# Kernel optimization log

Hardware: AMD Instinct MI355X
Metric: run time of the kernel (lower is better)

## Reference

```python
import jax, jax.numpy as jnp
import numpy as np

B, D, H, W = 1, 16, 16, 16
C, NH = 528, 8
HD = C // NH      # 66
K = 32            # retrieved memories per token


def setup_inputs() -> dict:
    key = jax.random.key(0)
    ks = jax.random.split(key, 4)
    x = jax.random.normal(ks[0], (B, D, H, W, C), jnp.float32)
    # simulated knn_memory.search output: (B, heads, N, K, 2[k/v], head_dim)
    knn_kv = jax.random.normal(ks[1], (B, NH, D * H * W, K, 2, HD), jnp.float32)
    w_qkv = jax.random.normal(ks[2], (3 * C, C), jnp.float32) * 0.02
    b_qkv = jnp.zeros((3 * C,), jnp.float32)
    w_proj = jax.random.normal(ks[3], (C, C), jnp.float32) * 0.02
    b_proj = jnp.zeros((C,), jnp.float32)
    return {"x": x, "knn_kv": knn_kv, "w_qkv": w_qkv, "b_qkv": b_qkv,
            "w_proj": w_proj, "b_proj": b_proj, "num_heads": NH}


def _l2norm(t):
    # F.normalize(t, dim=-1): t / max(||t||_2, eps)
    n = jnp.linalg.norm(t, axis=-1, keepdims=True)
    return t / jnp.maximum(n, 1e-12)


def _forward(x, knn_kv, w_qkv, b_qkv, w_proj, b_proj, num_heads):
    Bb, Dd, Hh, Ww, Cc = x.shape
    N = Dd * Hh * Ww
    hd = Cc // num_heads
    scaling = hd ** -0.5
    qkv = x.reshape(Bb * N, Cc) @ w_qkv.T + b_qkv
    qkv = qkv.reshape(Bb, N, 3, num_heads, hd).transpose(2, 0, 3, 1, 4)  # (3,B,h,N,hd)
    q, k, v = qkv[0], qkv[1], qkv[2]
    q = _l2norm(q)
    k = _l2norm(k)
    knn_k = knn_kv[..., 0, :]   # (B,h,N,K,hd)
    knn_v = knn_kv[..., 1, :]
    k_comb = jnp.concatenate([knn_k, k[..., None, :]], axis=-2)  # (B,h,N,K+1,hd)
    v_comb = jnp.concatenate([knn_v, v[..., None, :]], axis=-2)
    attn = jnp.einsum('bhnd,bhnkd->bhnk', q, k_comb) * scaling
    attn = jax.nn.softmax(attn, axis=-1)  # stable softmax
    out = jnp.einsum('bhnk,bhnkd->bhnd', attn, v_comb)  # (B,h,N,hd)
    out = out.transpose(0, 2, 1, 3).reshape(Bb * N, num_heads * hd)
    out = out @ w_proj.T + b_proj
    return out.reshape(Bb, Dd, Hh, Ww, Cc)


def reference(x, knn_kv, w_qkv, b_qkv, w_proj, b_proj, num_heads):
    return _forward(x, knn_kv, w_qkv, b_qkv, w_proj, b_proj, num_heads)
```

## Files before the change

kernel.cpp:

```cpp
#include <hip/hip_runtime.h>
#include <hip/hip_bf16.h>
#include <math.h>

#define N_POS 4096
#define C_DIM 528
#define NHEAD 8
#define HDIM  66
#define KNN   32
#define CQKV  1584
#define KP    544
#define NP1   1664
#define NP2   640

typedef __attribute__((ext_vector_type(8))) short short8;
typedef __attribute__((ext_vector_type(4))) float f32x4;
typedef __hip_bfloat16 bf16;

__global__ __launch_bounds__(256) void convpad3_kernel(
    const float* __restrict__ x, const float* __restrict__ wq,
    const float* __restrict__ wp,
    bf16* __restrict__ xb, bf16* __restrict__ wqb, bf16* __restrict__ wpb)
{
    int b = blockIdx.x;
    const float* src; bf16* dst; int Nr;
    if (b < N_POS)            { src = x;  dst = xb;  Nr = N_POS; }
    else if (b < N_POS + NP1) { b -= N_POS; src = wq; dst = wqb; Nr = CQKV; }
    else                      { b -= N_POS + NP1; src = wp; dst = wpb; Nr = C_DIM; }
    for (int c = threadIdx.x; c < KP; c += 256) {
        float v = (b < Nr && c < C_DIM) ? src[(size_t)b * C_DIM + c] : 0.0f;
        dst[(size_t)b * KP + c] = __float2bfloat16(v);
    }
}

__global__ __launch_bounds__(256) void gemm_mfma_kernel(
    const bf16* __restrict__ A, const bf16* __restrict__ B,
    const float* __restrict__ bias, float* __restrict__ C,
    int Nreal, int ldc)
{
    __shared__ short8 As[512];
    __shared__ short8 Bs[512];

    const int tid  = threadIdx.x;
    const int lane = tid & 63;
    const int wid  = tid >> 6;
    const int bm = blockIdx.y * 128;
    const int bn = blockIdx.x * 128;

    const int r0 = tid >> 2;
    const int c0 = tid & 3;
    const bf16* Ag = A + (size_t)(bm + r0) * KP + c0 * 8;
    const bf16* Bg = B + (size_t)(bn + r0) * KP + c0 * 8;
    const size_t roff = (size_t)64 * KP;

    short8 a0 = *(const short8*)(Ag);
    short8 a1 = *(const short8*)(Ag + roff);
    short8 b0 = *(const short8*)(Bg);
    short8 b1 = *(const short8*)(Bg + roff);

    const int w0 = r0 * 4 + (c0 ^ (r0 & 3));
    const int w1 = w0 + 256;

    const int wm = (wid >> 1) * 64;
    const int wn = (wid & 1) * 64;
    const int arow = wm + (lane & 15);
    const int brow = wn + (lane & 15);
    const int apc  = lane >> 4;
    const int aslot = arow * 4 + (apc ^ (arow & 3));
    const int bslot = brow * 4 + (apc ^ (brow & 3));

    f32x4 acc[4][4];
    #pragma unroll
    for (int i = 0; i < 4; ++i)
        #pragma unroll
        for (int j = 0; j < 4; ++j)
            acc[i][j] = (f32x4){0.f, 0.f, 0.f, 0.f};

    for (int k0 = 0;; k0 += 32) {
        As[w0] = a0; As[w1] = a1;
        Bs[w0] = b0; Bs[w1] = b1;
        __syncthreads();
        if (k0 + 32 < KP) {
            const bf16* An = Ag + (k0 + 32);
            const bf16* Bn = Bg + (k0 + 32);
            a0 = *(const short8*)(An);
            a1 = *(const short8*)(An + roff);
            b0 = *(const short8*)(Bn);
            b1 = *(const short8*)(Bn + roff);
        }
        short8 af[4], bfr[4];
        #pragma unroll
        for (int f = 0; f < 4; ++f) af[f]  = As[aslot + f * 64];
        #pragma unroll
        for (int f = 0; f < 4; ++f) bfr[f] = Bs[bslot + f * 64];
        #pragma unroll
        for (int i = 0; i < 4; ++i)
            #pragma unroll
            for (int j = 0; j < 4; ++j)
                acc[i][j] = __builtin_amdgcn_mfma_f32_16x16x32_bf16(
                    af[i], bfr[j], acc[i][j], 0, 0, 0);
        if (k0 + 32 >= KP) break;
        __syncthreads();
    }

    #pragma unroll
    for (int i = 0; i < 4; ++i) {
        const int row = bm + wm + i * 16 + (lane >> 4) * 4;
        #pragma unroll
        for (int j = 0; j < 4; ++j) {
            const int col = bn + wn + j * 16 + (lane & 15);
            if (col < Nreal) {
                const float bv = bias[col];
                #pragma unroll
                for (int r = 0; r < 4; ++r)
                    C[(size_t)(row + r) * ldc + col] = acc[i][j][r] + bv;
            }
        }
    }
}

__global__ __launch_bounds__(256) void attn_kernel(
    const float* __restrict__ qkv, const float* __restrict__ knn,
    bf16* __restrict__ out)
{
    const float scaling = 0.12309149097933272f;

    int bid = blockIdx.x;
    int h = bid >> 12;
    int n = bid & 4095;
    int tid = threadIdx.x;

    __shared__ float s_knn[KNN * 2 * HDIM];
    __shared__ float s_q[HDIM], s_k[HDIM], s_v[HDIM];
    __shared__ float s_dot[KNN + 1];
    __shared__ float s_scale[2];

    {
        const float4* src = (const float4*)(knn + ((size_t)bid) * (KNN * 2 * HDIM));
        float4* dst = (float4*)s_knn;
        for (int i = tid; i < KNN * 2 * HDIM / 4; i += 256) dst[i] = src[i];
    }
    const float* qp = qkv + (size_t)n * CQKV + h * HDIM;
    if (tid < HDIM) {
        s_q[tid] = qp[tid];
        s_k[tid] = qp[C_DIM + tid];
        s_v[tid] = qp[2 * C_DIM + tid];
    }
    __syncthreads();

    if (tid < 64) {
        float aq = s_q[tid] * s_q[tid];
        float ak = s_k[tid] * s_k[tid];
        if (tid < 2) {
            aq += s_q[64 + tid] * s_q[64 + tid];
            ak += s_k[64 + tid] * s_k[64 + tid];
        }
        #pragma unroll
        for (int off = 32; off; off >>= 1) {
            aq += __shfl_xor(aq, off);
            ak += __shfl_xor(ak, off);
        }
        if (tid == 0) {
            s_scale[0] = 1.0f / fmaxf(sqrtf(aq), 1e-12f);
            s_scale[1] = 1.0f / fmaxf(sqrtf(ak), 1e-12f);
        }
    }
    __syncthreads();
    if (tid < HDIM) {
        s_q[tid] *= s_scale[0];
        s_k[tid] *= s_scale[1];
    }
    __syncthreads();

    {
        int g = tid >> 3, l8 = tid & 7;
        float p = 0.f;
        for (int d = l8; d < HDIM; d += 8) p += s_q[d] * s_knn[g * (2 * HDIM) + d];
        p += __shfl_xor(p, 1);
        p += __shfl_xor(p, 2);
        p += __shfl_xor(p, 4);
        if (l8 == 0) s_dot[g] = p * scaling;
    }
    if (tid < 8) {
        float p = 0.f;
        for (int d = tid; d < HDIM; d += 8) p += s_q[d] * s_k[d];
        p += __shfl_xor(p, 1);
        p += __shfl_xor(p, 2);
        p += __shfl_xor(p, 4);
        if (tid == 0) s_dot[KNN] = p * scaling;
    }
    __syncthreads();

    if (tid < 64) {
        float x = (tid < 33) ? s_dot[tid] : -3.4e38f;
        float m = x;
        #pragma unroll
        for (int off = 32; off; off >>= 1) m = fmaxf(m, __shfl_xor(m, off));
        float e = (tid < 33) ? expf(x - m) : 0.f;
        float s = e;
        #pragma unroll
        for (int off = 32; off; off >>= 1) s += __shfl_xor(s, off);
        if (tid < 33) s_dot[tid] = e / s;
    }
    __syncthreads();

    if (tid < HDIM) {
        float acc = s_dot[KNN] * s_v[tid];
        #pragma unroll 8
        for (int k = 0; k < KNN; ++k)
            acc += s_dot[k] * s_knn[k * (2 * HDIM) + HDIM + tid];
        out[(size_t)n * KP + h * HDIM + tid] = __float2bfloat16(acc);
    }
    if (h == 0 && tid < KP - C_DIM) {
        out[(size_t)n * KP + C_DIM + tid] = __float2bfloat16(0.0f);
    }
}

extern "C" void kernel_launch(void* const* d_in, const int* in_sizes, int n_in,
                              void* d_out, int out_size, void* d_ws, size_t ws_size,
                              hipStream_t stream)
{
    const float* x      = (const float*)d_in[0];
    const float* knn_kv = (const float*)d_in[1];
    const float* w_qkv  = (const float*)d_in[2];
    const float* b_qkv  = (const float*)d_in[3];
    const float* w_proj = (const float*)d_in[4];
    const float* b_proj = (const float*)d_in[5];
    float* out = (float*)d_out;

    char* ws = (char*)d_ws;
    float* qkv = (float*)ws;
    bf16*  xb  = (bf16*)(ws + 25952256);
    bf16*  wqb = (bf16*)(ws + 25952256 + 4456448);
    bf16*  wpb = (bf16*)(ws + 25952256 + 4456448 + 1810432);
    bf16*  ab  = (bf16*)(ws + 25952256 + 4456448 + 1810432 + 696320);

    convpad3_kernel<<<N_POS + NP1 + NP2, 256, 0, stream>>>(x, w_qkv, w_proj, xb, wqb, wpb);

    gemm_mfma_kernel<<<dim3(NP1 / 128, N_POS / 128), 256, 0, stream>>>(
        xb, wqb, b_qkv, qkv, CQKV, CQKV);

    attn_kernel<<<dim3(NHEAD * N_POS), 256, 0, stream>>>(qkv, knn_kv, ab);

    gemm_mfma_kernel<<<dim3(NP2 / 128, N_POS / 128), 256, 0, stream>>>(
        ab, wpb, b_proj, out, C_DIM, C_DIM);
}
```

Baseline: 180.3 us.

## Process two tokens per attention block with register-staged KNN loads and fused normalization

Each attention block now handles two consecutive positions, with one 128-thread team per position, which halves the grid size. The KNN tile loads are issued into registers before being written to shared memory, so more loads are in flight at once. The L2 normalisation is folded algebraically into scale factors: the q·k dot, the norms and the local key dot are reduced in one wave while the other wave computes the raw q·knn dots. This drops one barrier and the pass that rescales q and k in place. It doubles shared memory per block and uses more registers, which may reduce occupancy.

```diff
diff --git a/kernel.cpp b/kernel.cpp
--- a/kernel.cpp
+++ b/kernel.cpp
@@ -124,94 +124,122 @@
 {
     const float scaling = 0.12309149097933272f;
 
-    int bid = blockIdx.x;
-    int h = bid >> 12;
-    int n = bid & 4095;
-    int tid = threadIdx.x;
-
-    __shared__ float s_knn[KNN * 2 * HDIM];
-    __shared__ float s_q[HDIM], s_k[HDIM], s_v[HDIM];
-    __shared__ float s_dot[KNN + 1];
-    __shared__ float s_scale[2];
-
-    {
-        const float4* src = (const float4*)(knn + ((size_t)bid) * (KNN * 2 * HDIM));
-        float4* dst = (float4*)s_knn;
-        for (int i = tid; i < KNN * 2 * HDIM / 4; i += 256) dst[i] = src[i];
-    }
-    const float* qp = qkv + (size_t)n * CQKV + h * HDIM;
-    if (tid < HDIM) {
-        s_q[tid] = qp[tid];
-        s_k[tid] = qp[C_DIM + tid];
-        s_v[tid] = qp[2 * C_DIM + tid];
+    const int bid = blockIdx.x;
+    const int tid = threadIdx.x;
+    const int g0  = bid << 1;
+    const int h   = g0 >> 12;
+    const int n0  = g0 & 4095;
+    const int n1  = n0 + 1;
+
+    __shared__ float s_knn[2][KNN * 132];
+    __shared__ float s_qkv[2][3 * HDIM];
+    __shared__ float s_dot[2][KNN + 1];
+    __shared__ float s_sc[2][2];
+
+    const float4* kb0 = (const float4*)(knn + (size_t)g0 * (KNN * 132));
+    const float4* kb1 = kb0 + KNN * 33;
+    float4 r0[4], r1[4];
+    float4 e0 = {0.f, 0.f, 0.f, 0.f}, e1 = {0.f, 0.f, 0.f, 0.f};
+    #pragma unroll
+    for (int i = 0; i < 4; ++i) r0[i] = kb0[tid + 256 * i];
+    if (tid < 32) e0 = kb0[1024 + tid];
+    #pragma unroll
+    for (int i = 0; i < 4; ++i) r1[i] = kb1[tid + 256 * i];
+    if (tid < 32) e1 = kb1[1024 + tid];
+
+    const float* qp0 = qkv + (size_t)n0 * CQKV + h * HDIM;
+    const float* qp1 = qp0 + CQKV;
+    float qv0 = 0.f, qv1 = 0.f;
+    int part = tid / HDIM, d66 = tid - part * HDIM;
+    if (tid < 3 * HDIM) {
+        qv0 = qp0[part * C_DIM + d66];
+        qv1 = qp1[part * C_DIM + d66];
+    }
+
+    float4* s40 = (float4*)s_knn[0];
+    float4* s41 = (float4*)s_knn[1];
+    #pragma unroll
+    for (int i = 0; i < 4; ++i) s40[tid + 256 * i] = r0[i];
+    if (tid < 32) s40[1024 + tid] = e0;
+    #pragma unroll
+    for (int i = 0; i < 4; ++i) s41[tid + 256 * i] = r1[i];
+    if (tid < 32) s41[1024 + tid] = e1;
+    if (tid < 3 * HDIM) {
+        s_qkv[0][tid] = qv0;
+        s_qkv[1][tid] = qv1;
     }
     __syncthreads();
 
-    if (tid < 64) {
-        float aq = s_q[tid] * s_q[tid];
-        float ak = s_k[tid] * s_k[tid];
-        if (tid < 2) {
-            aq += s_q[64 + tid] * s_q[64 + tid];
-            ak += s_k[64 + tid] * s_k[64 + tid];
+    const int team  = tid >> 7;
+    const int ttid  = tid & 127;
+    const int twave = ttid >> 6;
+    const int lane  = tid & 63;
+    const float* kK = s_knn[team];
+    const float* Q  = &s_qkv[team][0];
+    const float* KS = &s_qkv[team][HDIM];
+
+    if (twave == 0) {
+        const int j = lane >> 1, l2 = lane & 1;
+        const float* kr = kK + j * 132;
+        float p = 0.f;
+        #pragma unroll
+        for (int d = 0; d < HDIM / 2; ++d) p += Q[2 * d + l2] * kr[2 * d + l2];
+        p += __shfl_xor(p, 1);
+        if (l2 == 0) s_dot[team][j] = p;
+    } else {
+        float aq, ak, qk;
+        {
+            float qd = Q[lane], kd = KS[lane];
+            aq = qd * qd; ak = kd * kd; qk = qd * kd;
+            if (lane < 2) {
+                float q2 = Q[64 + lane], k2 = KS[64 + lane];
+                aq += q2 * q2; ak += k2 * k2; qk += q2 * k2;
+            }
         }
         #pragma unroll
         for (int off = 32; off; off >>= 1) {
             aq += __shfl_xor(aq, off);
             ak += __shfl_xor(ak, off);
-        }
-        if (tid == 0) {
-            s_scale[0] = 1.0f / fmaxf(sqrtf(aq), 1e-12f);
-            s_scale[1] = 1.0f / fmaxf(sqrtf(ak), 1e-12f);
+            qk += __shfl_xor(qk, off);
+        }
+        if (lane == 0) {
+            const float iq = 1.0f / fmaxf(sqrtf(aq), 1e-12f);
+            const float ik = 1.0f / fmaxf(sqrtf(ak), 1e-12f);
+            s_sc[team][0] = iq * scaling;
+            s_sc[team][1] = qk * iq * ik * scaling;
         }
     }
     __syncthreads();
-    if (tid < HDIM) {
-        s_q[tid] *= s_scale[0];
-        s_k[tid] *= s_scale[1];
+
+    if (twave == 0) {
+        float x = -3.4e38f;
+        if (lane < 32)       x = s_dot[team][lane] * s_sc[team][0];
+        else if (lane == 32) x = s_sc[team][1];
+        float m = x;
+        #pragma unroll
+        for (int off = 32; off; off >>= 1) m = fmaxf(m, __shfl_xor(m, off));
+        float e = (lane < 33) ? expf(x - m) : 0.f;
+        float s = e;
+        #pragma unroll
+        for (int off = 32; off; off >>= 1) s += __shfl_xor(s, off);
+        if (lane < 33) s_dot[team][lane] = e / s;
     }
     __syncthreads();
 
-    {
-        int g = tid >> 3, l8 = tid & 7;
-        float p = 0.f;
-        for (int d = l8; d < HDIM; d += 8) p += s_q[d] * s_knn[g * (2 * HDIM) + d];
-        p += __shfl_xor(p, 1);
-        p += __shfl_xor(p, 2);
-        p += __shfl_xor(p, 4);
-        if (l8 == 0) s_dot[g] = p * scaling;
-    }
-    if (tid < 8) {
-        float p = 0.f;
-        for (int d = tid; d < HDIM; d += 8) p += s_q[d] * s_k[d];
-        p += __shfl_xor(p, 1);
-        p += __shfl_xor(p, 2);
-        p += __shfl_xor(p, 4);
-        if (tid == 0) s_dot[KNN] = p * scaling;
-    }
-    __syncthreads();
-
-    if (tid < 64) {
-        float x = (tid < 33) ? s_dot[tid] : -3.4e38f;
-        float m = x;
-        #pragma unroll
-        for (int off = 32; off; off >>= 1) m = fmaxf(m, __shfl_xor(m, off));
-        float e = (tid < 33) ? expf(x - m) : 0.f;
-        float s = e;
-        #pragma unroll
-        for (int off = 32; off; off >>= 1) s += __shfl_xor(s, off);
-        if (tid < 33) s_dot[tid] = e / s;
-    }
-    __syncthreads();
-
-    if (tid < HDIM) {
-        float acc = s_dot[KNN] * s_v[tid];
+    if (ttid < HDIM) {
+        const int d = ttid;
+        float acc = s_dot[team][KNN] * s_qkv[team][2 * HDIM + d];
         #pragma unroll 8
-        for (int k = 0; k < KNN; ++k)
-            acc += s_dot[k] * s_knn[k * (2 * HDIM) + HDIM + tid];
-        out[(size_t)n * KP + h * HDIM + tid] = __float2bfloat16(acc);
-    }
-    if (h == 0 && tid < KP - C_DIM) {
-        out[(size_t)n * KP + C_DIM + tid] = __float2bfloat16(0.0f);
+        for (int j = 0; j < KNN; ++j)
+            acc += s_dot[team][j] * kK[j * 132 + HDIM + d];
+        const int n = team ? n1 : n0;
+        out[(size_t)n * KP + h * HDIM + d] = __float2bfloat16(acc);
+    }
+    if (h == 0) {
+        if (tid < 16)
+            out[(size_t)n0 * KP + C_DIM + tid] = __float2bfloat16(0.f);
+        else if (tid < 32)
+            out[(size_t)n1 * KP + C_DIM + (tid - 16)] = __float2bfloat16(0.f);
     }
 }
 
@@ -239,7 +267,7 @@
     gemm_mfma_kernel<<<dim3(NP1 / 128, N_POS / 128), 256, 0, stream>>>(
         xb, wqb, b_qkv, qkv, CQKV, CQKV);
 
-    attn_kernel<<<dim3(NHEAD * N_POS), 256, 0, stream>>>(qkv, knn_kv, ab);
+    attn_kernel<<<dim3(NHEAD * N_POS / 2), 256, 0, stream>>>(qkv, knn_kv, ab);
 
     gemm_mfma_kernel<<<dim3(NP2 / 128, N_POS / 128), 256, 0, stream>>>(
         ab, wpb, b_proj, out, C_DIM, C_DIM);
```

Result: faster. 171.0 us (-5.2%).
